# Performance work log

Hardware: AMD Instinct MI355X
Metric: run time of the kernel (lower is better)

The kernel has to match this reference:

```python
import jax, jax.numpy as jnp
import numpy as np

BATCH = 16384
MAX_ACTIVE = 32
FEAT = 768
HIDDEN = 1024


def setup_inputs() -> dict:
    key = jax.random.key(0)
    k1, k2, k3, k4, k5, k6 = jax.random.split(key, 6)
    stm = jax.random.randint(k1, (BATCH, MAX_ACTIVE), 0, FEAT, dtype=jnp.int32)
    nstm = jax.random.randint(k2, (BATCH, MAX_ACTIVE), 0, FEAT, dtype=jnp.int32)
    # Linear params (PyTorch layout: weight is (out_features, in_features))
    ft_w = jax.random.normal(k3, (HIDDEN, FEAT), dtype=jnp.float32) * 0.05
    ft_b = jax.random.normal(k4, (HIDDEN,), dtype=jnp.float32) * 0.05
    out_w = jax.random.normal(k5, (1, 2 * HIDDEN), dtype=jnp.float32) * 0.05
    out_b = jax.random.normal(k6, (1,), dtype=jnp.float32) * 0.05
    return {"stm": stm, "nstm": nstm, "ft_w": ft_w, "ft_b": ft_b,
            "out_w": out_w, "out_b": out_b}


def sparse_to_dense(indices: jnp.ndarray, size: int = FEAT) -> jnp.ndarray:
    """(B, max_active) int indices with -1 padding -> (B, size) 0/1 float32."""
    b = indices.shape[0]
    valid = (indices >= 0).astype(jnp.float32)          # (B, A)
    cols = jnp.clip(indices, 0, size - 1)               # padded -> col 0, masked by `valid`
    rows = jnp.arange(b, dtype=jnp.int32)[:, None]      # (B, 1) broadcast
    dense = jnp.zeros((b, size), dtype=jnp.float32)
    # .max matches torch's set-to-1 semantics even if duplicate indices occur
    return dense.at[rows, cols].max(valid)


def reference(stm, nstm, ft_w, ft_b, out_w, out_b):
    stm_d = sparse_to_dense(stm)                        # (B, 768)
    nstm_d = sparse_to_dense(nstm)                      # (B, 768)
    stm_h = stm_d @ ft_w.T + ft_b                       # (B, H)
    nstm_h = nstm_d @ ft_w.T + ft_b                     # (B, H)
    hidden = jnp.concatenate([stm_h, nstm_h], axis=1)   # (B, 2H)
    hidden = jnp.clip(hidden, 0.0, 1.0)
    return jax.nn.sigmoid(hidden @ out_w.T + out_b)     # (B, 1)
```

## Files before the change

### kernel.cpp

```cpp
#include <hip/hip_runtime.h>
#include <stdint.h>

#define BATCH 16384
#define MAXA 32
#define FEAT 768
#define HIDDEN 1024

__global__ __launch_bounds__(256) void prep_quant(const float* __restrict__ ftw,
                                                  uint8_t* __restrict__ wQ,
                                                  float* __restrict__ scale) {
  const int h0 = blockIdx.x * 8;
  const int hloc = threadIdx.x >> 5;
  const int l32 = threadIdx.x & 31;
  const int h = h0 + hloc;

  float w[24];
  float amax = 0.f;
  const float* __restrict__ src = ftw + (size_t)h * FEAT;
#pragma unroll
  for (int k = 0; k < 24; ++k) {
    w[k] = src[l32 + 32 * k];
    amax = fmaxf(amax, fabsf(w[k]));
  }
#pragma unroll
  for (int m = 1; m <= 16; m <<= 1)
    amax = fmaxf(amax, __shfl_xor(amax, m, 64));
  amax = fmaxf(amax, 1e-20f);
  if (l32 == 0) scale[h] = amax / 127.f;
  const float inv = 127.f / amax;

  __shared__ __align__(16) uint8_t tile[FEAT * 8];
#pragma unroll
  for (int k = 0; k < 24; ++k) {
    int q = __float2int_rn(w[k] * inv);
    tile[(l32 + 32 * k) * 8 + hloc] = (uint8_t)(q + 128);
  }
  __syncthreads();

#pragma unroll
  for (int p = 0; p < 3; ++p) {
    int f = threadIdx.x + 256 * p;
    unsigned long long v = *(const unsigned long long*)&tile[f * 8];
    *(unsigned long long*)(wQ + (size_t)f * HIDDEN + h0) = v;
  }

  if (blockIdx.x == 0)
    ((uint32_t*)(wQ + (size_t)FEAT * HIDDEN))[threadIdx.x] = 0x80808080u;
}

__device__ __forceinline__ void acc16(uint32_t* acc, uint4 w) {
  acc[0] += __builtin_amdgcn_perm(0u, w.x, 0x0c010c00u);
  acc[1] += __builtin_amdgcn_perm(0u, w.x, 0x0c030c02u);
  acc[2] += __builtin_amdgcn_perm(0u, w.y, 0x0c010c00u);
  acc[3] += __builtin_amdgcn_perm(0u, w.y, 0x0c030c02u);
  acc[4] += __builtin_amdgcn_perm(0u, w.z, 0x0c010c00u);
  acc[5] += __builtin_amdgcn_perm(0u, w.z, 0x0c030c02u);
  acc[6] += __builtin_amdgcn_perm(0u, w.w, 0x0c010c00u);
  acc[7] += __builtin_amdgcn_perm(0u, w.w, 0x0c030c02u);
}

__global__ __launch_bounds__(256, 3) void nn_fwd(
    const int* __restrict__ stm, const int* __restrict__ nstm,
    const uint8_t* __restrict__ wQ, const float* __restrict__ scale,
    const float* __restrict__ bias, const float* __restrict__ outw,
    const float* __restrict__ outb, float* __restrict__ out)
{
  const int lane = threadIdx.x & 63;
  const int row  = blockIdx.x * 4 + (threadIdx.x >> 6);
  const int half = lane >> 5;
  const int pos  = lane & 31;

  const int* __restrict__ src = half ? nstm : stm;
  int idx = src[row * MAXA + pos];
  bool valid = idx >= 0;
#pragma unroll
  for (int j = 0; j < 31; ++j) {
    int other = __shfl(idx, (half << 5) | j, 64);
    if (j < pos && other == idx) valid = false;
  }
  const int fmap = valid ? idx : FEAT;

  uint32_t accs[8], accn[8];
#pragma unroll
  for (int k = 0; k < 8; ++k) { accs[k] = 0u; accn[k] = 0u; }

  uint4 bs[8], bn[8];
#pragma unroll
  for (int j = 0; j < 8; ++j) {
    int fs_ = __builtin_amdgcn_readlane(fmap, j);
    int fn_ = __builtin_amdgcn_readlane(fmap, 32 + j);
    bs[j] = ((const uint4*)(wQ + (size_t)fs_ * HIDDEN))[lane];
    bn[j] = ((const uint4*)(wQ + (size_t)fn_ * HIDDEN))[lane];
  }
#pragma unroll
  for (int j = 0; j < 32; ++j) {
    uint4 ws_ = bs[j & 7];
    uint4 wn_ = bn[j & 7];
    if (j < 24) {
      int fs_ = __builtin_amdgcn_readlane(fmap, j + 8);
      int fn_ = __builtin_amdgcn_readlane(fmap, 32 + j + 8);
      bs[j & 7] = ((const uint4*)(wQ + (size_t)fs_ * HIDDEN))[lane];
      bn[j & 7] = ((const uint4*)(wQ + (size_t)fn_ * HIDDEN))[lane];
    }
    acc16(accs, ws_);
    acc16(accn, wn_);
  }

  const int DB = 32 * 128;

  const int hbase = lane * 16;
  float sc[16], bb[16], ows[16], own[16];
  {
    const float4* s4 = (const float4*)(scale + hbase);
    const float4* b4 = (const float4*)(bias + hbase);
    const float4* oS = (const float4*)(outw + hbase);
    const float4* oN = (const float4*)(outw + HIDDEN + hbase);
#pragma unroll
    for (int q = 0; q < 4; ++q) {
      float4 v;
      v = s4[q]; sc[4*q]=v.x; sc[4*q+1]=v.y; sc[4*q+2]=v.z; sc[4*q+3]=v.w;
      v = b4[q]; bb[4*q]=v.x; bb[4*q+1]=v.y; bb[4*q+2]=v.z; bb[4*q+3]=v.w;
      v = oS[q]; ows[4*q]=v.x; ows[4*q+1]=v.y; ows[4*q+2]=v.z; ows[4*q+3]=v.w;
      v = oN[q]; own[4*q]=v.x; own[4*q+1]=v.y; own[4*q+2]=v.z; own[4*q+3]=v.w;
    }
  }
  float partial = 0.f;
#pragma unroll
  for (int k = 0; k < 16; ++k) {
    uint32_t as = accs[k >> 1], an = accn[k >> 1];
    int qs = (int)((k & 1) ? (as >> 16) : (as & 0xffffu)) - DB;
    int qn = (int)((k & 1) ? (an >> 16) : (an & 0xffffu)) - DB;
    float hs = fminf(fmaxf(fmaf((float)qs, sc[k], bb[k]), 0.f), 1.f);
    float hn = fminf(fmaxf(fmaf((float)qn, sc[k], bb[k]), 0.f), 1.f);
    partial += hs * ows[k] + hn * own[k];
  }
#pragma unroll
  for (int off = 32; off > 0; off >>= 1)
    partial += __shfl_down(partial, off, 64);
  if (lane == 0) {
    float y = partial + outb[0];
    out[row] = 1.f / (1.f + __expf(-y));
  }
}

extern "C" void kernel_launch(void* const* d_in, const int* in_sizes, int n_in,
                              void* d_out, int out_size, void* d_ws, size_t ws_size,
                              hipStream_t stream) {
  const int*   stm  = (const int*)d_in[0];
  const int*   nstm = (const int*)d_in[1];
  const float* ftw  = (const float*)d_in[2];
  const float* ftb  = (const float*)d_in[3];
  const float* outw = (const float*)d_in[4];
  const float* outb = (const float*)d_in[5];

  uint8_t* wQ    = (uint8_t*)d_ws;
  float*   scale = (float*)(wQ + (size_t)(FEAT + 1) * HIDDEN);

  prep_quant<<<HIDDEN / 8, 256, 0, stream>>>(ftw, wQ, scale);
  nn_fwd<<<BATCH / 4, 256, 0, stream>>>(stm, nstm, wQ, scale, ftb, outw, outb,
                                        (float*)d_out);
}
```

Measured before the change: 117.2 us.

## Split each row's feature gather across two waves with LDS reduction

```diff
diff --git a/kernel.cpp b/kernel.cpp
--- a/kernel.cpp
+++ b/kernel.cpp
@@ -59,14 +59,17 @@
   acc[7] += __builtin_amdgcn_perm(0u, w.w, 0x0c030c02u);
 }
 
-__global__ __launch_bounds__(256, 3) void nn_fwd(
+__global__ __launch_bounds__(256, 4) void nn_fwd(
     const int* __restrict__ stm, const int* __restrict__ nstm,
     const uint8_t* __restrict__ wQ, const float* __restrict__ scale,
     const float* __restrict__ bias, const float* __restrict__ outw,
     const float* __restrict__ outb, float* __restrict__ out)
 {
   const int lane = threadIdx.x & 63;
-  const int row  = blockIdx.x * 4 + (threadIdx.x >> 6);
+  const int wid  = threadIdx.x >> 6;
+  const int rsel = wid >> 1;
+  const int fh16 = (wid & 1) * 16;
+  const int row  = blockIdx.x * 2 + rsel;
   const int half = lane >> 5;
   const int pos  = lane & 31;
 
@@ -84,26 +87,28 @@
 #pragma unroll
   for (int k = 0; k < 8; ++k) { accs[k] = 0u; accn[k] = 0u; }
 
-  uint4 bs[8], bn[8];
 #pragma unroll
-  for (int j = 0; j < 8; ++j) {
-    int fs_ = __builtin_amdgcn_readlane(fmap, j);
-    int fn_ = __builtin_amdgcn_readlane(fmap, 32 + j);
-    bs[j] = ((const uint4*)(wQ + (size_t)fs_ * HIDDEN))[lane];
-    bn[j] = ((const uint4*)(wQ + (size_t)fn_ * HIDDEN))[lane];
-  }
-#pragma unroll
-  for (int j = 0; j < 32; ++j) {
-    uint4 ws_ = bs[j & 7];
-    uint4 wn_ = bn[j & 7];
-    if (j < 24) {
-      int fs_ = __builtin_amdgcn_readlane(fmap, j + 8);
-      int fn_ = __builtin_amdgcn_readlane(fmap, 32 + j + 8);
-      bs[j & 7] = ((const uint4*)(wQ + (size_t)fs_ * HIDDEN))[lane];
-      bn[j & 7] = ((const uint4*)(wQ + (size_t)fn_ * HIDDEN))[lane];
-    }
+  for (int j = 0; j < 16; ++j) {
+    int fs_ = __builtin_amdgcn_readlane(fmap, fh16 + j);
+    int fn_ = __builtin_amdgcn_readlane(fmap, 32 + fh16 + j);
+    uint4 ws_ = ((const uint4*)(wQ + (size_t)fs_ * HIDDEN))[lane];
+    uint4 wn_ = ((const uint4*)(wQ + (size_t)fn_ * HIDDEN))[lane];
     acc16(accs, ws_);
     acc16(accn, wn_);
+  }
+
+  __shared__ __align__(16) uint32_t red[2][64][20];
+  if (fh16) {
+    uint32_t* r = &red[rsel][lane][0];
+#pragma unroll
+    for (int k = 0; k < 8; ++k) { r[k] = accs[k]; r[8 + k] = accn[k]; }
+  }
+  __syncthreads();
+  if (fh16) return;
+  {
+    const uint32_t* r = &red[rsel][lane][0];
+#pragma unroll
+    for (int k = 0; k < 8; ++k) { accs[k] += r[k]; accn[k] += r[8 + k]; }
   }
 
   const int DB = 32 * 128;
@@ -157,6 +162,6 @@
   float*   scale = (float*)(wQ + (size_t)(FEAT + 1) * HIDDEN);
 
   prep_quant<<<HIDDEN / 8, 256, 0, stream>>>(ftw, wQ, scale);
-  nn_fwd<<<BATCH / 4, 256, 0, stream>>>(stm, nstm, wQ, scale, ftb, outw, outb,
+  nn_fwd<<<BATCH / 2, 256, 0, stream>>>(stm, nstm, wQ, scale, ftb, outw, outb,
                                         (float*)d_out);
 }
```

New measurement: 290.9 us. +148.1%, slower.
